# Kernel tuning notes

Measured on AMD Instinct MI355X. Metric: run time of the kernel, lower is better.

Reference implementation:

```python
import jax, jax.numpy as jnp
import numpy as np

N_NODES = 5000
N_EDGES = 80000
HIDDEN = 128
NUM_RBF = 64
MAX_Z = 128
CUTOFF_UPPER = 5.0
LN_EPS = 1e-5


def setup_inputs() -> dict:
    key = jax.random.key(0)
    ks = jax.random.split(key, 24)
    H, R = HIDDEN, NUM_RBF
    def lin(k, out_d, in_d):
        s = 1.0 / np.sqrt(in_d)
        return jax.random.uniform(k, (out_d, in_d), jnp.float32, -s, s)
    def bias(k, out_d, in_d):
        s = 1.0 / np.sqrt(in_d)
        return jax.random.uniform(k, (out_d,), jnp.float32, -s, s)
    v = jax.random.normal(ks[3], (N_EDGES, 3), jnp.float32)
    v = v / jnp.linalg.norm(v, axis=-1, keepdims=True)
    return {
        "z": jax.random.randint(ks[0], (N_NODES,), 0, MAX_Z),
        "edge_index": jax.random.randint(ks[1], (2, N_EDGES), 0, N_NODES),
        "edge_weight": jax.random.uniform(ks[2], (N_EDGES,), jnp.float32) * CUTOFF_UPPER * 0.9,
        "edge_vec_norm": v,
        "edge_attr": jax.random.normal(ks[4], (N_EDGES, R), jnp.float32),
        "emb": jax.random.normal(ks[5], (MAX_Z, H), jnp.float32),
        "W_emb2": lin(ks[6], H, 2 * H), "b_emb2": bias(ks[7], H, 2 * H),
        "Wd1": lin(ks[8], H, R), "bd1": bias(ks[9], H, R),
        "Wd2": lin(ks[10], H, R), "bd2": bias(ks[11], H, R),
        "Wd3": lin(ks[12], H, R), "bd3": bias(ks[13], H, R),
        "Wt1": lin(ks[14], H, H), "Wt2": lin(ks[15], H, H), "Wt3": lin(ks[16], H, H),
        "Ws1": lin(ks[17], 2 * H, H), "bs1": bias(ks[18], 2 * H, H),
        "Ws2": lin(ks[19], 3 * H, 2 * H), "bs2": bias(ks[20], 3 * H, 2 * H),
        "ln_g": jnp.ones((H,), jnp.float32),
        "ln_b": jnp.zeros((H,), jnp.float32),
    }


def _skew(v):
    # v: [E,3] -> [E,3,3] skew-symmetric
    z = jnp.zeros_like(v[:, 0])
    return jnp.stack(
        [z, -v[:, 2], v[:, 1], v[:, 2], z, -v[:, 0], -v[:, 1], v[:, 0], z], axis=1
    ).reshape(-1, 3, 3)


def _sym(v):
    # symmetric traceless part of outer product (outer product already symmetric)
    outer = v[:, :, None] * v[:, None, :]
    tr = jnp.trace(outer, axis1=-2, axis2=-1) / 3.0
    return outer - tr[:, None, None] * jnp.eye(3, dtype=v.dtype)


def reference(z, edge_index, edge_weight, edge_vec_norm, edge_attr,
              emb, W_emb2, b_emb2, Wd1, bd1, Wd2, bd2, Wd3, bd3,
              Wt1, Wt2, Wt3, Ws1, bs1, Ws2, bs2, ln_g, ln_b):
    N = z.shape[0]
    H = emb.shape[1]
    src, dst = edge_index[0], edge_index[1]

    # atomic number message Zij: [E,H]
    Z = emb[z]
    Zij = jnp.concatenate([Z[src], Z[dst]], axis=-1) @ W_emb2.T + b_emb2

    # cosine cutoff (cutoff_lower = 0)
    cut = 0.5 * (jnp.cos(edge_weight * (jnp.pi / CUTOFF_UPPER)) + 1.0)
    cut = cut * (edge_weight < CUTOFF_UPPER).astype(edge_weight.dtype)
    C = cut[:, None] * Zij  # [E,H]

    f1 = (edge_attr @ Wd1.T + bd1) * C  # [E,H]
    f2 = (edge_attr @ Wd2.T + bd2) * C
    f3 = (edge_attr @ Wd3.T + bd3) * C

    eye = jnp.eye(3, dtype=C.dtype)
    Iij = f1[:, :, None, None] * eye  # [E,H,3,3]
    Aij = f2[:, :, None, None] * _skew(edge_vec_norm)[:, None, :, :]
    Sij = f3[:, :, None, None] * _sym(edge_vec_norm)[:, None, :, :]

    I = jax.ops.segment_sum(Iij, src, num_segments=N)  # [N,H,3,3]
    A = jax.ops.segment_sum(Aij, src, num_segments=N)
    S = jax.ops.segment_sum(Sij, src, num_segments=N)

    # Frobenius norm per channel, LayerNorm, scalar MLP
    tn = ((I + A + S) ** 2).sum((-2, -1))  # [N,H]
    mu = tn.mean(-1, keepdims=True)
    var = tn.var(-1, keepdims=True)
    norm = (tn - mu) / jnp.sqrt(var + LN_EPS) * ln_g + ln_b
    norm = jax.nn.silu(norm @ Ws1.T + bs1)
    norm = jax.nn.silu(norm @ Ws2.T + bs2)
    norm = norm.reshape(N, H, 3)

    I = jnp.einsum('nhij,gh->ngij', I, Wt1) * norm[:, :, 0, None, None]
    A = jnp.einsum('nhij,gh->ngij', A, Wt2) * norm[:, :, 1, None, None]
    S = jnp.einsum('nhij,gh->ngij', S, Wt3) * norm[:, :, 2, None, None]
    return I + A + S
```

## Files before the change

### kernel.cpp

```cpp
#include <hip/hip_runtime.h>
#include <hip/hip_bf16.h>

#define NN   5000
#define NP   5008
#define NE   80000
#define HID  128
#define NRBF 64
#define PI_OVER_5 0.6283185307179586f
#define LN_EPS 1e-5f

typedef unsigned short bf16_t;
typedef __attribute__((ext_vector_type(8))) short short8;
typedef __attribute__((ext_vector_type(4))) float floatx4;

__device__ __forceinline__ bf16_t to_bf16(float x){
    union { float f; unsigned int u; } v; v.f = x;
    unsigned int r = v.u + 0x7fffu + ((v.u >> 16) & 1u);
    return (bf16_t)(r >> 16);
}
__device__ __forceinline__ float from_bf16(bf16_t h){
    union { unsigned int u; float f; } v; v.u = ((unsigned int)h) << 16;
    return v.f;
}
__device__ __forceinline__ uint4 pack8(const float* s){
    float4 a = *(const float4*)s;
    float4 b = *(const float4*)(s + 4);
    uint4 o;
    o.x = to_bf16(a.x) | ((unsigned)to_bf16(a.y) << 16);
    o.y = to_bf16(a.z) | ((unsigned)to_bf16(a.w) << 16);
    o.z = to_bf16(b.x) | ((unsigned)to_bf16(b.y) << 16);
    o.w = to_bf16(b.z) | ((unsigned)to_bf16(b.w) << 16);
    return o;
}

__global__ __launch_bounds__(128) void k_embtab(
    const float* __restrict__ W_emb2, const float* __restrict__ emb,
    float* __restrict__ embL, float* __restrict__ embR)
{
    int t = blockIdx.x;
    int h = threadIdx.x;
    const float* er = emb + t * HID;
    const float* wl = W_emb2 + (size_t)h * (2 * HID);
    float sl = 0.f, sr = 0.f;
    #pragma unroll 8
    for (int k = 0; k < HID; k++){
        float e = er[k];
        sl += wl[k] * e;
        sr += wl[HID + k] * e;
    }
    embL[t * HID + h] = sl;
    embR[t * HID + h] = sr;
}

__global__ __launch_bounds__(256) void k_prep_wts(
    const float* __restrict__ Wd1, const float* __restrict__ Wd2, const float* __restrict__ Wd3,
    const float* __restrict__ bd1, const float* __restrict__ bd2, const float* __restrict__ bd3,
    const float* __restrict__ Wt1, const float* __restrict__ Wt2, const float* __restrict__ Wt3,
    const float* __restrict__ Ws1, const float* __restrict__ Ws2,
    bf16_t* __restrict__ Wcat, bf16_t* __restrict__ Wtc,
    bf16_t* __restrict__ Ws1b, bf16_t* __restrict__ Ws2b, float* __restrict__ bdcat)
{
    int t = blockIdx.x * 256 + threadIdx.x;
    int i8 = t * 8;
    const float* src; bf16_t* dst;
    if (i8 < 24576){
        int j = i8; int tb = j >> 13; int r = j & 8191;
        src = ((tb == 0) ? Wd1 : (tb == 1) ? Wd2 : Wd3) + r; dst = Wcat + j;
    } else if (i8 < 24576 + 49152){
        int j = i8 - 24576; int tb = j >> 14; int r = j & 16383;
        src = ((tb == 0) ? Wt1 : (tb == 1) ? Wt2 : Wt3) + r; dst = Wtc + j;
    } else if (i8 < 24576 + 49152 + 32768){
        int j = i8 - 73728; src = Ws1 + j; dst = Ws1b + j;
    } else {
        int j = i8 - 106496; src = Ws2 + j; dst = Ws2b + j;
    }
    *(uint4*)dst = pack8(src);
    if (t < 384){
        int tb2 = t >> 7, ch2 = t & 127;
        const float* bsrc = (tb2 == 0) ? bd1 : ((tb2 == 1) ? bd2 : bd3);
        bdcat[t] = bsrc[ch2];
    }
}

__global__ void k_count(const int* __restrict__ ei, int* __restrict__ counts){
    int e = blockIdx.x * 256 + threadIdx.x;
    if (e < NE) atomicAdd(&counts[ei[e]], 1);
}

__global__ __launch_bounds__(1024) void k_scan(
    const int* __restrict__ counts, int* __restrict__ offsets, int* __restrict__ cursor)
{
    __shared__ int s[1024];
    const int t = threadIdx.x;
    const int CH = 5;
    int base = t * CH;
    int loc[CH];
    int lsum = 0;
    #pragma unroll
    for (int u = 0; u < CH; u++){
        int i = base + u;
        int v = (i < NN) ? counts[i] : 0;
        loc[u] = lsum;
        lsum += v;
    }
    s[t] = lsum;
    __syncthreads();
    for (int d = 1; d < 1024; d <<= 1){
        int v = (t >= d) ? s[t - d] : 0;
        __syncthreads();
        s[t] += v;
        __syncthreads();
    }
    int excl = s[t] - lsum;
    #pragma unroll
    for (int u = 0; u < CH; u++){
        int i = base + u;
        if (i < NN){ int o = excl + loc[u]; offsets[i] = o; cursor[i] = o; }
    }
    if (t == 1023) offsets[NN] = s[1023];
}

__global__ void k_fill(const int* __restrict__ ei, const int* __restrict__ z,
                       const float* __restrict__ ew, const float* __restrict__ evn,
                       int* __restrict__ cursor, int* __restrict__ elist,
                       float2* __restrict__ meta, float* __restrict__ evn_p){
    int e = blockIdx.x * 256 + threadIdx.x;
    if (e < NE){
        int sN = ei[e], dN = ei[NE + e];
        int p = atomicAdd(&cursor[sN], 1);
        elist[p] = e;
        float w = ew[e];
        float c = (w < 5.0f) ? 0.5f * (__cosf(w * PI_OVER_5) + 1.0f) : 0.0f;
        meta[p] = make_float2(c, __int_as_float(z[sN] | (z[dN] << 8)));
        evn_p[p*3+0] = evn[e*3+0];
        evn_p[p*3+1] = evn[e*3+1];
        evn_p[p*3+2] = evn[e*3+2];
    }
}

__global__ __launch_bounds__(256) void k_edge(
    const float* __restrict__ attr, const int* __restrict__ elist,
    const float2* __restrict__ meta,
    const bf16_t* __restrict__ Wcat, const float* __restrict__ bdcat,
    const float* __restrict__ embL, const float* __restrict__ embR,
    const float* __restrict__ b_emb2,
    bf16_t* __restrict__ f1, bf16_t* __restrict__ f2, bf16_t* __restrict__ f3)
{
    __shared__ __align__(16) bf16_t sB[64 * 72];
    __shared__ float sCut[64];
    __shared__ int   sZ[64];

    const int tid = threadIdx.x;
    const int p0  = blockIdx.x * 64;

    {
        int r = tid >> 2, qt = tid & 3;
        int e = elist[p0 + r];
        const float* ar = attr + (size_t)e * NRBF + qt * 16;
        uint4 o0 = pack8(ar);
        uint4 o1 = pack8(ar + 8);
        *(uint4*)&sB[r * 72 + qt * 16]     = o0;
        *(uint4*)&sB[r * 72 + qt * 16 + 8] = o1;
    }
    if (tid < 64){
        float2 m = meta[p0 + tid];
        sCut[tid] = m.x;
        sZ[tid]   = __float_as_int(m.y);
    }
    __syncthreads();

    const int wv = tid >> 6, lane = tid & 63;
    const int col = lane & 15, q = lane >> 4;

    floatx4 acc[6][4];
    #pragma unroll
    for (int mt = 0; mt < 6; mt++)
        #pragma unroll
        for (int nt = 0; nt < 4; nt++)
            acc[mt][nt] = (floatx4)(0.f);

    #pragma unroll
    for (int s = 0; s < 2; s++){
        short8 bf[4];
        #pragma unroll
        for (int nt = 0; nt < 4; nt++){
            int r = nt * 16 + col;
            bf[nt] = *(const short8*)&sB[r * 72 + s * 32 + q * 8];
        }
        short8 af[6];
        #pragma unroll
        for (int t = 0; t < 3; t++)
            #pragma unroll
            for (int c = 0; c < 2; c++){
                int m = t * 128 + wv * 32 + c * 16 + col;
                af[t * 2 + c] = *(const short8*)(Wcat + (size_t)m * NRBF + s * 32 + q * 8);
            }
        #pragma unroll
        for (int mt = 0; mt < 6; mt++)
            #pragma unroll
            for (int nt = 0; nt < 4; nt++)
                acc[mt][nt] = __builtin_amdgcn_mfma_f32_16x16x32_bf16(
                    af[mt], bf[nt], acc[mt][nt], 0, 0, 0);
    }

    floatx4 be[2], bd[3][2];
    #pragma unroll
    for (int c = 0; c < 2; c++){
        int ch4 = wv * 32 + c * 16 + q * 4;
        be[c] = *(const floatx4*)(b_emb2 + ch4);
        #pragma unroll
        for (int t = 0; t < 3; t++)
            bd[t][c] = *(const floatx4*)(bdcat + t * 128 + ch4);
    }
    bf16_t* const fs[3] = {f1, f2, f3};
    #pragma unroll
    for (int nt = 0; nt < 4; nt++){
        int e = nt * 16 + col;
        float cut = sCut[e];
        int zp = sZ[e];
        int zs = zp & 255, zd = zp >> 8;
        size_t orow = (size_t)(p0 + e) * HID;
        #pragma unroll
        for (int c = 0; c < 2; c++){
            int ch4 = wv * 32 + c * 16 + q * 4;
            floatx4 L = *(const floatx4*)(embL + zs * HID + ch4);
            floatx4 R = *(const floatx4*)(embR + zd * HID + ch4);
            floatx4 Cv = (L + R + be[c]) * cut;
            #pragma unroll
            for (int t = 0; t < 3; t++){
                floatx4 v = (acc[t * 2 + c][nt] + bd[t][c]) * Cv;
                uint2 pk;
                pk.x = to_bf16(v[0]) | ((unsigned)to_bf16(v[1]) << 16);
                pk.y = to_bf16(v[2]) | ((unsigned)to_bf16(v[3]) << 16);
                *(uint2*)(fs[t] + orow + ch4) = pk;
            }
        }
    }
}

__global__ __launch_bounds__(128) void k_gather(
    const int* __restrict__ offsets, const float* __restrict__ evn_p,
    const bf16_t* __restrict__ f1, const bf16_t* __restrict__ f2, const bf16_t* __restrict__ f3,
    const float* __restrict__ ln_g, const float* __restrict__ ln_b,
    bf16_t* __restrict__ acc, bf16_t* __restrict__ ln_out)
{
    const int n = blockIdx.x, h = threadIdx.x;
    const int s = offsets[n], e_end = offsets[n + 1];
    float c=0, ax=0, ay=0, az=0, sxx=0, syy=0, szz=0, sxy=0, sxz=0, syz=0;
    for (int idx = s; idx < e_end; idx++){
        float vx = evn_p[idx*3+0], vy = evn_p[idx*3+1], vz = evn_p[idx*3+2];
        float t3 = (vx*vx + vy*vy + vz*vz) * (1.f/3.f);
        float a = from_bf16(f1[(size_t)idx * HID + h]);
        float b = from_bf16(f2[(size_t)idx * HID + h]);
        float d = from_bf16(f3[(size_t)idx * HID + h]);
        c += a;
        ax += b * vx; ay += b * vy; az += b * vz;
        sxx += d * (vx*vx - t3); syy += d * (vy*vy - t3); szz += d * (vz*vz - t3);
        sxy += d * (vx*vy); sxz += d * (vx*vz); syz += d * (vy*vz);
    }
    const int PS = NP * HID;
    const int base = n * HID + h;
    acc[0*PS+base]=to_bf16(c);   acc[1*PS+base]=to_bf16(ax);
    acc[2*PS+base]=to_bf16(ay);  acc[3*PS+base]=to_bf16(az);
    acc[4*PS+base]=to_bf16(sxx); acc[5*PS+base]=to_bf16(syy);
    acc[6*PS+base]=to_bf16(szz); acc[7*PS+base]=to_bf16(sxy);
    acc[8*PS+base]=to_bf16(sxz); acc[9*PS+base]=to_bf16(syz);

    float tn = 3.f*c*c + 2.f*c*(sxx+syy+szz)
             + sxx*sxx + syy*syy + szz*szz
             + 2.f*(sxy*sxy + sxz*sxz + syz*syz)
             + 2.f*(ax*ax + ay*ay + az*az);

    __shared__ float r1[128], r2[128];
    r1[h] = tn; r2[h] = tn * tn;
    __syncthreads();
    for (int st = 64; st > 0; st >>= 1){
        if (h < st){ r1[h] += r1[h + st]; r2[h] += r2[h + st]; }
        __syncthreads();
    }
    float mu  = r1[0] * (1.f / HID);
    float var = r2[0] * (1.f / HID) - mu * mu;
    ln_out[base] = to_bf16((tn - mu) * rsqrtf(var + LN_EPS) * ln_g[h] + ln_b[h]);
}

__global__ __launch_bounds__(256) void k_node(
    const bf16_t* __restrict__ lnb, const bf16_t* __restrict__ accb,
    const bf16_t* __restrict__ Ws1b, const float* __restrict__ bs1,
    const bf16_t* __restrict__ Ws2b, const float* __restrict__ bs2,
    const bf16_t* __restrict__ Wtc,
    float* __restrict__ out)
{
    __shared__ __align__(16) bf16_t h1s[16 * 280];
    __shared__ float nrms[16 * 392];

    const int tid = threadIdx.x;
    const int wv = tid >> 6, lane = tid & 63;
    const int col = lane & 15, q = lane >> 4;
    const int n0 = blockIdx.x * 16;

    {
        short8 a1[4];
        #pragma unroll
        for (int k = 0; k < 4; k++)
            a1[k] = *(const short8*)(lnb + (size_t)(n0 + col) * HID + k * 32 + q * 8);
        floatx4 c1[4];
        #pragma unroll
        for (int nt = 0; nt < 4; nt++) c1[nt] = (floatx4)(0.f);
        #pragma unroll
        for (int nt = 0; nt < 4; nt++){
            int cg = wv * 64 + nt * 16 + col;
            #pragma unroll
            for (int k = 0; k < 4; k++){
                short8 b = *(const short8*)(Ws1b + (size_t)cg * HID + k * 32 + q * 8);
                c1[nt] = __builtin_amdgcn_mfma_f32_16x16x32_bf16(a1[k], b, c1[nt], 0, 0, 0);
            }
        }
        #pragma unroll
        for (int nt = 0; nt < 4; nt++){
            int cg = wv * 64 + nt * 16 + col;
            float bias = bs1[cg];
            #pragma unroll
            for (int r = 0; r < 4; r++){
                float v = c1[nt][r] + bias;
                v = v / (1.f + __expf(-v));
                h1s[(q * 4 + r) * 280 + cg] = to_bf16(v);
            }
        }
    }
    __syncthreads();

    {
        short8 a2[8];
        #pragma unroll
        for (int k = 0; k < 8; k++)
            a2[k] = *(const short8*)&h1s[col * 280 + k * 32 + q * 8];
        floatx4 c2[6];
        #pragma unroll
        for (int nt = 0; nt < 6; nt++) c2[nt] = (floatx4)(0.f);
        #pragma unroll
        for (int nt = 0; nt < 6; nt++){
            int cg = wv * 96 + nt * 16 + col;
            #pragma unroll
            for (int k = 0; k < 8; k++){
                short8 b = *(const short8*)(Ws2b + (size_t)cg * 256 + k * 32 + q * 8);
                c2[nt] = __builtin_amdgcn_mfma_f32_16x16x32_bf16(a2[k], b, c2[nt], 0, 0, 0);
            }
        }
        #pragma unroll
        for (int nt = 0; nt < 6; nt++){
            int cg = wv * 96 + nt * 16 + col;
            float bias = bs2[cg];
            #pragma unroll
            for (int r = 0; r < 4; r++){
                float v = c2[nt][r] + bias;
                v = v / (1.f + __expf(-v));
                nrms[(q * 4 + r) * 392 + cg] = v;
            }
        }
    }
    __syncthreads();

    floatx4 cm[10][2];
    #pragma unroll
    for (int p = 0; p < 10; p++){
        #pragma unroll
        for (int nt = 0; nt < 2; nt++) cm[p][nt] = (floatx4)(0.f);
    }
    #pragma unroll
    for (int p = 0; p < 10; p++){
        const bf16_t* ap = accb + (size_t)p * NP * HID + (size_t)(n0 + col) * HID;
        short8 a3[4];
        #pragma unroll
        for (int k = 0; k < 4; k++)
            a3[k] = *(const short8*)(ap + k * 32 + q * 8);
        int tb = (p == 0) ? 0 : ((p < 4) ? 1 : 2);
        #pragma unroll
        for (int nt = 0; nt < 2; nt++){
            int g = wv * 32 + nt * 16 + col;
            const bf16_t* wp = Wtc + tb * 16384 + (size_t)g * HID;
            #pragma unroll
            for (int k = 0; k < 4; k++){
                short8 b = *(const short8*)(wp + k * 32 + q * 8);
                cm[p][nt] = __builtin_amdgcn_mfma_f32_16x16x32_bf16(a3[k], b, cm[p][nt], 0, 0, 0);
            }
        }
    }
    #pragma unroll
    for (int nt = 0; nt < 2; nt++){
        int g = wv * 32 + nt * 16 + col;
        #pragma unroll
        for (int r = 0; r < 4; r++){
            int node = q * 4 + r;
            int n = n0 + node;
            if (n < NN){
                float n0f = nrms[node * 392 + g * 3 + 0];
                float n1f = nrms[node * 392 + g * 3 + 1];
                float n2f = nrms[node * 392 + g * 3 + 2];
                float c   = cm[0][nt][r];
                float ax  = cm[1][nt][r], ay = cm[2][nt][r], az = cm[3][nt][r];
                float sxx = cm[4][nt][r], syy= cm[5][nt][r], szz= cm[6][nt][r];
                float sxy = cm[7][nt][r], sxz= cm[8][nt][r], syz= cm[9][nt][r];
                float* o = out + ((size_t)n * HID + g) * 9;
                o[0] = n0f*c + n2f*sxx;   o[1] = n2f*sxy - n1f*az;  o[2] = n2f*sxz + n1f*ay;
                o[3] = n2f*sxy + n1f*az;  o[4] = n0f*c + n2f*syy;   o[5] = n2f*syz - n1f*ax;
                o[6] = n2f*sxz - n1f*ay;  o[7] = n2f*syz + n1f*ax;  o[8] = n0f*c + n2f*szz;
            }
        }
    }
}

extern "C" void kernel_launch(void* const* d_in, const int* in_sizes, int n_in,
                              void* d_out, int out_size, void* d_ws, size_t ws_size,
                              hipStream_t stream)
{
    (void)in_sizes; (void)n_in; (void)out_size; (void)ws_size;
    const int*   z      = (const int*)  d_in[0];
    const int*   ei     = (const int*)  d_in[1];
    const float* ew     = (const float*)d_in[2];
    const float* evn    = (const float*)d_in[3];
    const float* attr   = (const float*)d_in[4];
    const float* emb    = (const float*)d_in[5];
    const float* W_emb2 = (const float*)d_in[6];
    const float* b_emb2 = (const float*)d_in[7];
    const float* Wd1 = (const float*)d_in[8];  const float* bd1 = (const float*)d_in[9];
    const float* Wd2 = (const float*)d_in[10]; const float* bd2 = (const float*)d_in[11];
    const float* Wd3 = (const float*)d_in[12]; const float* bd3 = (const float*)d_in[13];
    const float* Wt1 = (const float*)d_in[14]; const float* Wt2 = (const float*)d_in[15];
    const float* Wt3 = (const float*)d_in[16];
    const float* Ws1 = (const float*)d_in[17]; const float* bs1 = (const float*)d_in[18];
    const float* Ws2 = (const float*)d_in[19]; const float* bs2 = (const float*)d_in[20];
    const float* ln_g = (const float*)d_in[21]; const float* ln_b = (const float*)d_in[22];
    float* out = (float*)d_out;

    char* ws = (char*)d_ws;
    size_t o = 0;
    auto take = [&](size_t b)->size_t{ size_t c = o; o += (b + 255) & ~(size_t)255; return c; };
    size_t f1_o  = take((size_t)NE * HID * 2);
    size_t f2_o  = take((size_t)NE * HID * 2);
    size_t f3_o  = take((size_t)NE * HID * 2);
    size_t acc_o = take((size_t)10 * NP * HID * 2);
    size_t ln_of = take((size_t)NP * HID * 2);
    size_t eL_o  = take((size_t)128 * HID * 4);
    size_t eR_o  = take((size_t)128 * HID * 4);
    size_t cnt_o = take((size_t)NN * 4);
    size_t off_o = take((size_t)(NN + 1) * 4);
    size_t cur_o = take((size_t)NN * 4);
    size_t el_o  = take((size_t)NE * 4);
    size_t met_o = take((size_t)NE * 8);
    size_t evp_o = take((size_t)NE * 12);
    size_t wc_o  = take((size_t)384 * 64 * 2);
    size_t wt_o  = take((size_t)3 * 128 * 128 * 2);
    size_t w1_o  = take((size_t)256 * 128 * 2);
    size_t w2_o  = take((size_t)384 * 256 * 2);
    size_t bdc_o = take((size_t)384 * 4);

    bf16_t* f1 = (bf16_t*)(ws + f1_o);
    bf16_t* f2 = (bf16_t*)(ws + f2_o);
    bf16_t* f3 = (bf16_t*)(ws + f3_o);
    bf16_t* accb = (bf16_t*)(ws + acc_o);
    bf16_t* lnb  = (bf16_t*)(ws + ln_of);
    float* embL = (float*)(ws + eL_o);
    float* embR = (float*)(ws + eR_o);
    int* counts = (int*)(ws + cnt_o);
    int* offs   = (int*)(ws + off_o);
    int* cursor = (int*)(ws + cur_o);
    int* elist  = (int*)(ws + el_o);
    float2* meta = (float2*)(ws + met_o);
    float* evn_p = (float*)(ws + evp_o);
    bf16_t* Wcat = (bf16_t*)(ws + wc_o);
    bf16_t* Wtc  = (bf16_t*)(ws + wt_o);
    bf16_t* Ws1b = (bf16_t*)(ws + w1_o);
    bf16_t* Ws2b = (bf16_t*)(ws + w2_o);
    float* bdcat = (float*)(ws + bdc_o);

    hipMemsetAsync(counts, 0, (size_t)NN * 4, stream);

    k_prep_wts<<<100, 256, 0, stream>>>(Wd1, Wd2, Wd3, bd1, bd2, bd3,
                                        Wt1, Wt2, Wt3, Ws1, Ws2,
                                        Wcat, Wtc, Ws1b, Ws2b, bdcat);
    k_embtab<<<128, 128, 0, stream>>>(W_emb2, emb, embL, embR);
    k_count <<<(NE + 255) / 256, 256, 0, stream>>>(ei, counts);
    k_scan  <<<1, 1024, 0, stream>>>(counts, offs, cursor);
    k_fill  <<<(NE + 255) / 256, 256, 0, stream>>>(ei, z, ew, evn, cursor, elist, meta, evn_p);
    k_edge  <<<NE / 64, 256, 0, stream>>>(attr, elist, meta, Wcat, bdcat,
                                          embL, embR, b_emb2, f1, f2, f3);
    k_gather<<<NN, 128, 0, stream>>>(offs, evn_p, f1, f2, f3, ln_g, ln_b, accb, lnb);
    k_node  <<<(NN + 15) / 16, 256, 0, stream>>>(lnb, accb, Ws1b, bs1, Ws2b, bs2, Wtc, out);
}
```

Baseline: 229.8 us.

## Fuse edge MFMA filter computation into per-node gather, drop f1/f2/f3 buffers

Merges the edge filter GEMM kernel and the per-node segment-sum gather into one kernel with one block per node. Each block computes the RBF projections with MFMA for its own CSR edges and accumulates the ten tensor components straight into registers. This removes the write and read-back of the three bf16 edge feature arrays (about 60 MB of traffic). The embedding-table kernel is also folded into the weight-prep kernel to save a launch. In exchange, each node block loads all weight fragments into registers and runs partial 16-edge tiles, which wastes MFMA work for nodes with few edges and adds register pressure.

After: 242.3 us. +5.4%, slower.

```diff
diff --git a/kernel.cpp b/kernel.cpp
--- a/kernel.cpp
+++ b/kernel.cpp
@@ -32,53 +32,57 @@
     o.w = to_bf16(b.z) | ((unsigned)to_bf16(b.w) << 16);
     return o;
 }
-
-__global__ __launch_bounds__(128) void k_embtab(
-    const float* __restrict__ W_emb2, const float* __restrict__ emb,
-    float* __restrict__ embL, float* __restrict__ embR)
-{
-    int t = blockIdx.x;
-    int h = threadIdx.x;
-    const float* er = emb + t * HID;
-    const float* wl = W_emb2 + (size_t)h * (2 * HID);
-    float sl = 0.f, sr = 0.f;
-    #pragma unroll 8
-    for (int k = 0; k < HID; k++){
-        float e = er[k];
-        sl += wl[k] * e;
-        sr += wl[HID + k] * e;
-    }
-    embL[t * HID + h] = sl;
-    embR[t * HID + h] = sr;
-}
-
-__global__ __launch_bounds__(256) void k_prep_wts(
+__device__ __forceinline__ short8 cvt8(float4 a, float4 b){
+    short8 r;
+    r[0] = (short)to_bf16(a.x); r[1] = (short)to_bf16(a.y);
+    r[2] = (short)to_bf16(a.z); r[3] = (short)to_bf16(a.w);
+    r[4] = (short)to_bf16(b.x); r[5] = (short)to_bf16(b.y);
+    r[6] = (short)to_bf16(b.z); r[7] = (short)to_bf16(b.w);
+    return r;
+}
+
+__global__ __launch_bounds__(256) void k_prep(
     const float* __restrict__ Wd1, const float* __restrict__ Wd2, const float* __restrict__ Wd3,
     const float* __restrict__ bd1, const float* __restrict__ bd2, const float* __restrict__ bd3,
     const float* __restrict__ Wt1, const float* __restrict__ Wt2, const float* __restrict__ Wt3,
     const float* __restrict__ Ws1, const float* __restrict__ Ws2,
+    const float* __restrict__ W_emb2, const float* __restrict__ emb,
     bf16_t* __restrict__ Wcat, bf16_t* __restrict__ Wtc,
-    bf16_t* __restrict__ Ws1b, bf16_t* __restrict__ Ws2b, float* __restrict__ bdcat)
+    bf16_t* __restrict__ Ws1b, bf16_t* __restrict__ Ws2b, float* __restrict__ bdcat,
+    float* __restrict__ embL, float* __restrict__ embR)
 {
-    int t = blockIdx.x * 256 + threadIdx.x;
-    int i8 = t * 8;
-    const float* src; bf16_t* dst;
-    if (i8 < 24576){
-        int j = i8; int tb = j >> 13; int r = j & 8191;
-        src = ((tb == 0) ? Wd1 : (tb == 1) ? Wd2 : Wd3) + r; dst = Wcat + j;
-    } else if (i8 < 24576 + 49152){
-        int j = i8 - 24576; int tb = j >> 14; int r = j & 16383;
-        src = ((tb == 0) ? Wt1 : (tb == 1) ? Wt2 : Wt3) + r; dst = Wtc + j;
-    } else if (i8 < 24576 + 49152 + 32768){
-        int j = i8 - 73728; src = Ws1 + j; dst = Ws1b + j;
+    int b = blockIdx.x, tid = threadIdx.x;
+    if (b < 100){
+        int t = b * 256 + tid;
+        int i8 = t * 8;
+        const float* src; bf16_t* dst;
+        if (i8 < 24576){
+            int j = i8; int tb = j >> 13; int r = j & 8191;
+            src = ((tb == 0) ? Wd1 : (tb == 1) ? Wd2 : Wd3) + r; dst = Wcat + j;
+        } else if (i8 < 24576 + 49152){
+            int j = i8 - 24576; int tb = j >> 14; int r = j & 16383;
+            src = ((tb == 0) ? Wt1 : (tb == 1) ? Wt2 : Wt3) + r; dst = Wtc + j;
+        } else if (i8 < 24576 + 49152 + 32768){
+            int j = i8 - 73728; src = Ws1 + j; dst = Ws1b + j;
+        } else {
+            int j = i8 - 106496; src = Ws2 + j; dst = Ws2b + j;
+        }
+        *(uint4*)dst = pack8(src);
+        if (t < 384){
+            int tb2 = t >> 7, ch2 = t & 127;
+            const float* bsrc = (tb2 == 0) ? bd1 : ((tb2 == 1) ? bd2 : bd3);
+            bdcat[t] = bsrc[ch2];
+        }
     } else {
-        int j = i8 - 106496; src = Ws2 + j; dst = Ws2b + j;
-    }
-    *(uint4*)dst = pack8(src);
-    if (t < 384){
-        int tb2 = t >> 7, ch2 = t & 127;
-        const float* bsrc = (tb2 == 0) ? bd1 : ((tb2 == 1) ? bd2 : bd3);
-        bdcat[t] = bsrc[ch2];
+        int t = b - 100;
+        int half = tid >> 7;
+        int h = tid & 127;
+        const float* wl = W_emb2 + (size_t)h * (2 * HID) + half * HID;
+        const float* er = emb + t * HID;
+        float s = 0.f;
+        #pragma unroll 8
+        for (int k = 0; k < HID; k++) s += wl[k] * er[k];
+        (half ? embR : embL)[t * HID + h] = s;
     }
 }
 
@@ -138,149 +142,158 @@
     }
 }
 
-__global__ __launch_bounds__(256) void k_edge(
-    const float* __restrict__ attr, const int* __restrict__ elist,
-    const float2* __restrict__ meta,
+__global__ __launch_bounds__(256) void k_edge_gather(
+    const int* __restrict__ offs, const int* __restrict__ elist,
+    const float2* __restrict__ meta, const float* __restrict__ evn_p,
+    const float* __restrict__ attr,
     const bf16_t* __restrict__ Wcat, const float* __restrict__ bdcat,
     const float* __restrict__ embL, const float* __restrict__ embR,
     const float* __restrict__ b_emb2,
-    bf16_t* __restrict__ f1, bf16_t* __restrict__ f2, bf16_t* __restrict__ f3)
+    const float* __restrict__ ln_g, const float* __restrict__ ln_b,
+    bf16_t* __restrict__ accb, bf16_t* __restrict__ lnb)
 {
-    __shared__ __align__(16) bf16_t sB[64 * 72];
-    __shared__ float sCut[64];
-    __shared__ int   sZ[64];
+    __shared__ __align__(16) float4 sV[64];
+    __shared__ int   sZZ[64];
+    __shared__ float sAcc[10][132];
+    __shared__ float sRed[8];
 
     const int tid = threadIdx.x;
-    const int p0  = blockIdx.x * 64;
-
-    {
-        int r = tid >> 2, qt = tid & 3;
-        int e = elist[p0 + r];
-        const float* ar = attr + (size_t)e * NRBF + qt * 16;
-        uint4 o0 = pack8(ar);
-        uint4 o1 = pack8(ar + 8);
-        *(uint4*)&sB[r * 72 + qt * 16]     = o0;
-        *(uint4*)&sB[r * 72 + qt * 16 + 8] = o1;
-    }
-    if (tid < 64){
-        float2 m = meta[p0 + tid];
-        sCut[tid] = m.x;
-        sZ[tid]   = __float_as_int(m.y);
-    }
-    __syncthreads();
-
     const int wv = tid >> 6, lane = tid & 63;
     const int col = lane & 15, q = lane >> 4;
-
-    floatx4 acc[6][4];
-    #pragma unroll
-    for (int mt = 0; mt < 6; mt++)
-        #pragma unroll
-        for (int nt = 0; nt < 4; nt++)
-            acc[mt][nt] = (floatx4)(0.f);
-
-    #pragma unroll
-    for (int s = 0; s < 2; s++){
-        short8 bf[4];
-        #pragma unroll
-        for (int nt = 0; nt < 4; nt++){
-            int r = nt * 16 + col;
-            bf[nt] = *(const short8*)&sB[r * 72 + s * 32 + q * 8];
-        }
-        short8 af[6];
-        #pragma unroll
-        for (int t = 0; t < 3; t++)
-            #pragma unroll
-            for (int c = 0; c < 2; c++){
-                int m = t * 128 + wv * 32 + c * 16 + col;
-                af[t * 2 + c] = *(const short8*)(Wcat + (size_t)m * NRBF + s * 32 + q * 8);
-            }
-        #pragma unroll
-        for (int mt = 0; mt < 6; mt++)
-            #pragma unroll
-            for (int nt = 0; nt < 4; nt++)
-                acc[mt][nt] = __builtin_amdgcn_mfma_f32_16x16x32_bf16(
-                    af[mt], bf[nt], acc[mt][nt], 0, 0, 0);
-    }
-
-    floatx4 be[2], bd[3][2];
-    #pragma unroll
-    for (int c = 0; c < 2; c++){
-        int ch4 = wv * 32 + c * 16 + q * 4;
-        be[c] = *(const floatx4*)(b_emb2 + ch4);
-        #pragma unroll
-        for (int t = 0; t < 3; t++)
-            bd[t][c] = *(const floatx4*)(bdcat + t * 128 + ch4);
-    }
-    bf16_t* const fs[3] = {f1, f2, f3};
-    #pragma unroll
-    for (int nt = 0; nt < 4; nt++){
-        int e = nt * 16 + col;
-        float cut = sCut[e];
-        int zp = sZ[e];
-        int zs = zp & 255, zd = zp >> 8;
-        size_t orow = (size_t)(p0 + e) * HID;
-        #pragma unroll
-        for (int c = 0; c < 2; c++){
-            int ch4 = wv * 32 + c * 16 + q * 4;
-            floatx4 L = *(const floatx4*)(embL + zs * HID + ch4);
-            floatx4 R = *(const floatx4*)(embR + zd * HID + ch4);
-            floatx4 Cv = (L + R + be[c]) * cut;
-            #pragma unroll
-            for (int t = 0; t < 3; t++){
-                floatx4 v = (acc[t * 2 + c][nt] + bd[t][c]) * Cv;
-                uint2 pk;
-                pk.x = to_bf16(v[0]) | ((unsigned)to_bf16(v[1]) << 16);
-                pk.y = to_bf16(v[2]) | ((unsigned)to_bf16(v[3]) << 16);
-                *(uint2*)(fs[t] + orow + ch4) = pk;
-            }
-        }
-    }
-}
-
-__global__ __launch_bounds__(128) void k_gather(
-    const int* __restrict__ offsets, const float* __restrict__ evn_p,
-    const bf16_t* __restrict__ f1, const bf16_t* __restrict__ f2, const bf16_t* __restrict__ f3,
-    const float* __restrict__ ln_g, const float* __restrict__ ln_b,
-    bf16_t* __restrict__ acc, bf16_t* __restrict__ ln_out)
-{
-    const int n = blockIdx.x, h = threadIdx.x;
-    const int s = offsets[n], e_end = offsets[n + 1];
-    float c=0, ax=0, ay=0, az=0, sxx=0, syy=0, szz=0, sxy=0, sxz=0, syz=0;
-    for (int idx = s; idx < e_end; idx++){
-        float vx = evn_p[idx*3+0], vy = evn_p[idx*3+1], vz = evn_p[idx*3+2];
-        float t3 = (vx*vx + vy*vy + vz*vz) * (1.f/3.f);
-        float a = from_bf16(f1[(size_t)idx * HID + h]);
-        float b = from_bf16(f2[(size_t)idx * HID + h]);
-        float d = from_bf16(f3[(size_t)idx * HID + h]);
-        c += a;
-        ax += b * vx; ay += b * vy; az += b * vz;
-        sxx += d * (vx*vx - t3); syy += d * (vy*vy - t3); szz += d * (vz*vz - t3);
-        sxy += d * (vx*vy); sxz += d * (vx*vz); syz += d * (vy*vz);
-    }
-    const int PS = NP * HID;
-    const int base = n * HID + h;
-    acc[0*PS+base]=to_bf16(c);   acc[1*PS+base]=to_bf16(ax);
-    acc[2*PS+base]=to_bf16(ay);  acc[3*PS+base]=to_bf16(az);
-    acc[4*PS+base]=to_bf16(sxx); acc[5*PS+base]=to_bf16(syy);
-    acc[6*PS+base]=to_bf16(szz); acc[7*PS+base]=to_bf16(sxy);
-    acc[8*PS+base]=to_bf16(sxz); acc[9*PS+base]=to_bf16(syz);
-
-    float tn = 3.f*c*c + 2.f*c*(sxx+syy+szz)
-             + sxx*sxx + syy*syy + szz*szz
-             + 2.f*(sxy*sxy + sxz*sxz + syz*syz)
-             + 2.f*(ax*ax + ay*ay + az*az);
-
-    __shared__ float r1[128], r2[128];
-    r1[h] = tn; r2[h] = tn * tn;
+    const int n = blockIdx.x;
+    const int s = offs[n], e_end = offs[n + 1];
+
+    short8 bfr[6][2];
+    float bdv[3][2], bev[2];
+    #pragma unroll
+    for (int cg = 0; cg < 2; cg++){
+        int ch = wv * 32 + cg * 16 + col;
+        bev[cg] = b_emb2[ch];
+        #pragma unroll
+        for (int t = 0; t < 3; t++){
+            bdv[t][cg] = bdcat[t * 128 + ch];
+            #pragma unroll
+            for (int s2 = 0; s2 < 2; s2++)
+                bfr[t * 2 + cg][s2] = *(const short8*)(Wcat + (size_t)(t * 128 + ch) * NRBF + s2 * 32 + q * 8);
+        }
+    }
+
+    float pl[10][2];
+    #pragma unroll
+    for (int p = 0; p < 10; p++){ pl[p][0] = 0.f; pl[p][1] = 0.f; }
+
+    for (int c0 = s; c0 < e_end; c0 += 64){
+        __syncthreads();
+        if (tid < 64){
+            int pos = c0 + tid;
+            if (pos < e_end){
+                float2 m = meta[pos];
+                sV[tid]  = make_float4(evn_p[pos*3+0], evn_p[pos*3+1], evn_p[pos*3+2], m.x);
+                sZZ[tid] = __float_as_int(m.y);
+            } else {
+                sV[tid]  = make_float4(0.f, 0.f, 0.f, 0.f);
+                sZZ[tid] = 0;
+            }
+        }
+        __syncthreads();
+        int nch = e_end - c0; if (nch > 64) nch = 64;
+        int ntiles = (nch + 15) >> 4;
+        for (int t16 = 0; t16 < ntiles; t16++){
+            int pos = c0 + t16 * 16 + col;
+            int cpos = (pos < e_end) ? pos : (e_end - 1);
+            int e = elist[cpos];
+            const float* ar = attr + (size_t)e * NRBF + q * 8;
+            short8 af[2];
+            #pragma unroll
+            for (int s2 = 0; s2 < 2; s2++){
+                float4 u0 = *(const float4*)(ar + s2 * 32);
+                float4 u1 = *(const float4*)(ar + s2 * 32 + 4);
+                af[s2] = cvt8(u0, u1);
+            }
+            floatx4 D[3][2];
+            #pragma unroll
+            for (int t = 0; t < 3; t++)
+                #pragma unroll
+                for (int cg = 0; cg < 2; cg++){
+                    floatx4 d = (floatx4)(0.f);
+                    d = __builtin_amdgcn_mfma_f32_16x16x32_bf16(af[0], bfr[t*2+cg][0], d, 0, 0, 0);
+                    d = __builtin_amdgcn_mfma_f32_16x16x32_bf16(af[1], bfr[t*2+cg][1], d, 0, 0, 0);
+                    D[t][cg] = d;
+                }
+            #pragma unroll
+            for (int r = 0; r < 4; r++){
+                int eslot = t16 * 16 + q * 4 + r;
+                float4 vv = sV[eslot];
+                int zp = sZZ[eslot];
+                int zs = zp & 255, zd = zp >> 8;
+                float vx = vv.x, vy = vv.y, vz = vv.z, cut = vv.w;
+                float xx = vx*vx, yy = vy*vy, zz = vz*vz;
+                float t3 = (xx + yy + zz) * (1.f/3.f);
+                float gxx = xx - t3, gyy = yy - t3, gzz = zz - t3;
+                float gxy = vx*vy, gxz = vx*vz, gyz = vy*vz;
+                #pragma unroll
+                for (int cg = 0; cg < 2; cg++){
+                    int ch = wv * 32 + cg * 16 + col;
+                    float L = embL[zs * HID + ch];
+                    float R = embR[zd * HID + ch];
+                    float Cv = cut * (L + R + bev[cg]);
+                    float f1 = (D[0][cg][r] + bdv[0][cg]) * Cv;
+                    float f2 = (D[1][cg][r] + bdv[1][cg]) * Cv;
+                    float f3 = (D[2][cg][r] + bdv[2][cg]) * Cv;
+                    pl[0][cg] += f1;
+                    pl[1][cg] += f2 * vx; pl[2][cg] += f2 * vy; pl[3][cg] += f2 * vz;
+                    pl[4][cg] += f3 * gxx; pl[5][cg] += f3 * gyy; pl[6][cg] += f3 * gzz;
+                    pl[7][cg] += f3 * gxy; pl[8][cg] += f3 * gxz; pl[9][cg] += f3 * gyz;
+                }
+            }
+        }
+    }
+
+    #pragma unroll
+    for (int p = 0; p < 10; p++)
+        #pragma unroll
+        for (int cg = 0; cg < 2; cg++){
+            float v = pl[p][cg];
+            v += __shfl_xor(v, 16);
+            v += __shfl_xor(v, 32);
+            pl[p][cg] = v;
+        }
+    if (lane < 16){
+        #pragma unroll
+        for (int p = 0; p < 10; p++){
+            sAcc[p][wv * 32 + 0  + lane] = pl[p][0];
+            sAcc[p][wv * 32 + 16 + lane] = pl[p][1];
+        }
+    }
     __syncthreads();
-    for (int st = 64; st > 0; st >>= 1){
-        if (h < st){ r1[h] += r1[h + st]; r2[h] += r2[h + st]; }
-        __syncthreads();
-    }
-    float mu  = r1[0] * (1.f / HID);
-    float var = r2[0] * (1.f / HID) - mu * mu;
-    ln_out[base] = to_bf16((tn - mu) * rsqrtf(var + LN_EPS) * ln_g[h] + ln_b[h]);
+
+    float av[10]; float tn = 0.f;
+    const int ch = tid;
+    if (tid < 128){
+        #pragma unroll
+        for (int p = 0; p < 10; p++) av[p] = sAcc[p][ch];
+        tn = 3.f*av[0]*av[0] + 2.f*av[0]*(av[4]+av[5]+av[6])
+           + av[4]*av[4] + av[5]*av[5] + av[6]*av[6]
+           + 2.f*(av[7]*av[7] + av[8]*av[8] + av[9]*av[9])
+           + 2.f*(av[1]*av[1] + av[2]*av[2] + av[3]*av[3]);
+    }
+    float s1 = tn, s2 = tn * tn;
+    #pragma unroll
+    for (int d = 1; d < 64; d <<= 1){
+        s1 += __shfl_xor(s1, d);
+        s2 += __shfl_xor(s2, d);
+    }
+    if (lane == 0){ sRed[wv] = s1; sRed[4 + wv] = s2; }
+    __syncthreads();
+    if (tid < 128){
+        float mu  = (sRed[0] + sRed[1]) * (1.f / HID);
+        float var = (sRed[4] + sRed[5]) * (1.f / HID) - mu * mu;
+        float ln = (tn - mu) * rsqrtf(var + LN_EPS) * ln_g[ch] + ln_b[ch];
+        lnb[(size_t)n * HID + ch] = to_bf16(ln);
+        #pragma unroll
+        for (int p = 0; p < 10; p++)
+            accb[(size_t)p * NP * HID + (size_t)n * HID + ch] = to_bf16(av[p]);
+    }
 }
 
 __global__ __launch_bounds__(256) void k_node(
@@ -435,9 +448,6 @@
     char* ws = (char*)d_ws;
     size_t o = 0;
     auto take = [&](size_t b)->size_t{ size_t c = o; o += (b + 255) & ~(size_t)255; return c; };
-    size_t f1_o  = take((size_t)NE * HID * 2);
-    size_t f2_o  = take((size_t)NE * HID * 2);
-    size_t f3_o  = take((size_t)NE * HID * 2);
     size_t acc_o = take((size_t)10 * NP * HID * 2);
     size_t ln_of = take((size_t)NP * HID * 2);
     size_t eL_o  = take((size_t)128 * HID * 4);
@@ -454,9 +464,6 @@
     size_t w2_o  = take((size_t)384 * 256 * 2);
     size_t bdc_o = take((size_t)384 * 4);
 
-    bf16_t* f1 = (bf16_t*)(ws + f1_o);
-    bf16_t* f2 = (bf16_t*)(ws + f2_o);
-    bf16_t* f3 = (bf16_t*)(ws + f3_o);
     bf16_t* accb = (bf16_t*)(ws + acc_o);
     bf16_t* lnb  = (bf16_t*)(ws + ln_of);
     float* embL = (float*)(ws + eL_o);
@@ -475,15 +482,14 @@
 
     hipMemsetAsync(counts, 0, (size_t)NN * 4, stream);
 
-    k_prep_wts<<<100, 256, 0, stream>>>(Wd1, Wd2, Wd3, bd1, bd2, bd3,
-                                        Wt1, Wt2, Wt3, Ws1, Ws2,
-                                        Wcat, Wtc, Ws1b, Ws2b, bdcat);
-    k_embtab<<<128, 128, 0, stream>>>(W_emb2, emb, embL, embR);
-    k_count <<<(NE + 255) / 256, 256, 0, stream>>>(ei, counts);
-    k_scan  <<<1, 1024, 0, stream>>>(counts, offs, cursor);
-    k_fill  <<<(NE + 255) / 256, 256, 0, stream>>>(ei, z, ew, evn, cursor, elist, meta, evn_p);
-    k_edge  <<<NE / 64, 256, 0, stream>>>(attr, elist, meta, Wcat, bdcat,
-                                          embL, embR, b_emb2, f1, f2, f3);
-    k_gather<<<NN, 128, 0, stream>>>(offs, evn_p, f1, f2, f3, ln_g, ln_b, accb, lnb);
-    k_node  <<<(NN + 15) / 16, 256, 0, stream>>>(lnb, accb, Ws1b, bs1, Ws2b, bs2, Wtc, out);
-}
+    k_prep <<<228, 256, 0, stream>>>(Wd1, Wd2, Wd3, bd1, bd2, bd3,
+                                     Wt1, Wt2, Wt3, Ws1, Ws2, W_emb2, emb,
+                                     Wcat, Wtc, Ws1b, Ws2b, bdcat, embL, embR);
+    k_count<<<(NE + 255) / 256, 256, 0, stream>>>(ei, counts);
+    k_scan <<<1, 1024, 0, stream>>>(counts, offs, cursor);
+    k_fill <<<(NE + 255) / 256, 256, 0, stream>>>(ei, z, ew, evn, cursor, elist, meta, evn_p);
+    k_edge_gather<<<NN, 256, 0, stream>>>(offs, elist, meta, evn_p, attr,
+                                          Wcat, bdcat, embL, embR, b_emb2,
+                                          ln_g, ln_b, accb, lnb);
+    k_node <<<(NN + 15) / 16, 256, 0, stream>>>(lnb, accb, Ws1b, bs1, Ws2b, bs2, Wtc, out);
+}
```
